# Optimization experiments

Hardware: AMD Instinct MI355X
Metric: run time of the kernel (lower is better)

Reference implementation:

```python
import jax, jax.numpy as jnp
import numpy as np

IN_F = 175
HID = 1024
OUT_F = 175


def setup_inputs() -> dict:
    key = jax.random.key(0)
    ks = jax.random.split(key, 16)
    B, T = 128, 200
    s = 0.02
    w = lambda k, shape: (jax.random.normal(k, shape, jnp.float32) * s)
    return {
        "real_seq": jax.random.normal(ks[0], (B, T, IN_F), jnp.float32),
        "W_ih1": w(ks[1], (4 * HID, IN_F)), "W_hh1": w(ks[2], (4 * HID, HID)),
        "b_ih1": w(ks[3], (4 * HID,)), "b_hh1": w(ks[4], (4 * HID,)),
        "W_ih2": w(ks[5], (4 * HID, HID)), "W_hh2": w(ks[6], (4 * HID, HID)),
        "b_ih2": w(ks[7], (4 * HID,)), "b_hh2": w(ks[8], (4 * HID,)),
        "W_ih3": w(ks[9], (4 * HID, HID)), "W_hh3": w(ks[10], (4 * HID, HID)),
        "b_ih3": w(ks[11], (4 * HID,)), "b_hh3": w(ks[12], (4 * HID,)),
        "W_dec": w(ks[13], (OUT_F, HID)), "b_dec": w(ks[14], (OUT_F,)),
    }


def _condition_mask(seq_len, condition_num=5, groundtruth_num=5):
    gt = np.ones((100, groundtruth_num))
    con = np.zeros((100, condition_num))
    lst = np.concatenate((gt, con), 1).reshape(-1)[:seq_len]
    return jnp.asarray(lst.astype(bool))


def _lstm_cell(x, h, c, Wih, Whh, bih, bhh):
    # PyTorch LSTMCell: gate order i, f, g, o
    gates = x @ Wih.T + h @ Whh.T + bih + bhh
    i, f, g, o = jnp.split(gates, 4, axis=-1)
    c_new = jax.nn.sigmoid(f) * c + jax.nn.sigmoid(i) * jnp.tanh(g)
    h_new = jax.nn.sigmoid(o) * jnp.tanh(c_new)
    return h_new, c_new


def reference(real_seq, W_ih1, W_hh1, b_ih1, b_hh1,
              W_ih2, W_hh2, b_ih2, b_hh2,
              W_ih3, W_hh3, b_ih3, b_hh3,
              W_dec, b_dec):
    B, T, _ = real_seq.shape
    H = W_hh1.shape[1]
    Fo = W_dec.shape[0]
    cond = _condition_mask(T)
    z = jnp.zeros((B, H), real_seq.dtype)
    carry0 = (z, z, z, z, z, z, jnp.zeros((B, Fo), real_seq.dtype))

    def step(carry, xs):
        h0, h1, h2, c0, c1, c2, out_frame = carry
        x_t, use_gt = xs
        in_frame = jnp.where(use_gt, x_t, out_frame)
        nh0, nc0 = _lstm_cell(in_frame, h0, c0, W_ih1, W_hh1, b_ih1, b_hh1)
        # NOTE: source feeds the PREVIOUS h0 / h1 to layers 2 / 3 (faithful)
        nh1, nc1 = _lstm_cell(h0, h1, c1, W_ih2, W_hh2, b_ih2, b_hh2)
        nh2, nc2 = _lstm_cell(h1, h2, c2, W_ih3, W_hh3, b_ih3, b_hh3)
        out = nh2 @ W_dec.T + b_dec
        return (nh0, nh1, nh2, nc0, nc1, nc2, out), out

    _, outs = jax.lax.scan(step, carry0,
                           (jnp.transpose(real_seq, (1, 0, 2)), cond))
    # [T, B, Fo] -> [B, T*Fo] (matches torch.cat along dim 1 per step)
    return jnp.transpose(outs, (1, 0, 2)).reshape(B, T * Fo)
```

## Files before the change

kernel.cpp:

```cpp
#include <hip/hip_runtime.h>

#define B_ 128
#define T_ 200
#define INF_ 175
#define INFP_ 192
#define H_ 1024
#define G4_ 4096
#define OUTF_ 175
#define BH3_ (3 * B_ * H_)
#define NCELL 192
#define NDEC 22
#define NWORK (NCELL + NDEC)
#define NBLK (NWORK + 1)
#define SP 16

typedef __bf16 bf16x8 __attribute__((ext_vector_type(8)));
typedef float f32x4 __attribute__((ext_vector_type(4)));

__device__ __attribute__((aligned(16))) __bf16 g_Wih1p[G4_ * INFP_];
__device__ __attribute__((aligned(16))) __bf16 g_Whh1[G4_ * H_];
__device__ __attribute__((aligned(16))) __bf16 g_Wih2[G4_ * H_];
__device__ __attribute__((aligned(16))) __bf16 g_Whh2[G4_ * H_];
__device__ __attribute__((aligned(16))) __bf16 g_Wih3[G4_ * H_];
__device__ __attribute__((aligned(16))) __bf16 g_Whh3[G4_ * H_];
__device__ __attribute__((aligned(16))) __bf16 g_Wdec[OUTF_ * H_];
__device__ float g_bsum[3 * G4_];
__device__ float g_bdec[OUTF_];
__device__ __attribute__((aligned(16))) __bf16 g_h[2][BH3_];
__device__ __attribute__((aligned(16))) __bf16 g_infp[B_ * INFP_];
__device__ __attribute__((aligned(16))) __bf16 g_xp[(long)T_ * B_ * INFP_];
__device__ int g_isf32;
__device__ int g_flags[256 * SP];
__device__ int g_dflags[32 * SP];
__device__ int g_gen8[8 * SP];
__device__ int g_iready8[8 * SP];

__device__ __forceinline__ f32x4 mfma_bf16(bf16x8 a, bf16x8 b, f32x4 c) {
    return __builtin_amdgcn_mfma_f32_16x16x32_bf16(a, b, c, 0, 0, 0);
}
__device__ __forceinline__ bf16x8 ld8(const __bf16* p) {
    return *reinterpret_cast<const bf16x8*>(p);
}
__device__ __forceinline__ float sigm(float x) { return 1.f / (1.f + expf(-x)); }
__device__ __forceinline__ float rdf(const void* p, long i, int f32) {
    return f32 ? ((const float*)p)[i] : (float)((const __bf16*)p)[i];
}
__device__ __forceinline__ unsigned short bf2u(__bf16 v) {
    union { __bf16 b; unsigned short u; } c; c.b = v; return c.u;
}

__device__ __forceinline__ void lds_barrier() {
    asm volatile("s_waitcnt lgkmcnt(0)" ::: "memory");
    __builtin_amdgcn_s_barrier();
}

__device__ __forceinline__ void spin_rmw(int* addr, int target, int iters) {
    for (int it = 0; it < iters; ++it) {
        if (__hip_atomic_fetch_max(addr, 0, __ATOMIC_RELAXED, __HIP_MEMORY_SCOPE_AGENT) >= target)
            break;
        __builtin_amdgcn_s_sleep(1);
    }
    (void)__hip_atomic_load(addr, __ATOMIC_ACQUIRE, __HIP_MEMORY_SCOPE_AGENT);
}

__global__ void detect_k(const unsigned int* __restrict__ xw) {
    __shared__ int cnt;
    if (threadIdx.x == 0) cnt = 0;
    __syncthreads();
    unsigned int w = xw[threadIdx.x];
    int e = (w >> 7) & 0xFF;
    if (e >= 140) atomicAdd(&cnt, 1);
    __syncthreads();
    if (threadIdx.x == 0) g_isf32 = (cnt >= 16) ? 1 : 0;
}

__global__ void prep_k(const void* Wih1, const void* Whh1, const void* Wih2,
                       const void* Whh2, const void* Wih3, const void* Whh3,
                       const void* Wdec, const void* bih1, const void* bhh1,
                       const void* bih2, const void* bhh2, const void* bih3,
                       const void* bhh3, const void* bdec, const void* xseq) {
    const int f = g_isf32;
    const int idx = blockIdx.x * 256 + threadIdx.x;
    const int stride = gridDim.x * 256;
    if (idx < 256 * SP) g_flags[idx] = 0;
    if (idx < 32 * SP) g_dflags[idx] = 0;
    if (idx < 8 * SP) { g_gen8[idx] = 0; g_iready8[idx] = 0; }
    for (int i = idx; i < G4_ * INFP_; i += stride) {
        int n = i / INFP_, k = i - n * INFP_;
        g_Wih1p[i] = (k < INF_) ? (__bf16)rdf(Wih1, (long)n * INF_ + k, f) : (__bf16)0.f;
    }
    for (int i = idx; i < G4_ * H_; i += stride) {
        g_Whh1[i] = (__bf16)rdf(Whh1, i, f);
        g_Wih2[i] = (__bf16)rdf(Wih2, i, f);
        g_Whh2[i] = (__bf16)rdf(Whh2, i, f);
        g_Wih3[i] = (__bf16)rdf(Wih3, i, f);
        g_Whh3[i] = (__bf16)rdf(Whh3, i, f);
    }
    for (int i = idx; i < OUTF_ * H_; i += stride) g_Wdec[i] = (__bf16)rdf(Wdec, i, f);
    for (int i = idx; i < G4_; i += stride) {
        g_bsum[i]           = rdf(bih1, i, f) + rdf(bhh1, i, f);
        g_bsum[G4_ + i]     = rdf(bih2, i, f) + rdf(bhh2, i, f);
        g_bsum[2 * G4_ + i] = rdf(bih3, i, f) + rdf(bhh3, i, f);
    }
    for (int i = idx; i < OUTF_; i += stride) g_bdec[i] = rdf(bdec, i, f);
    for (int i = idx; i < 2 * BH3_; i += stride) (&g_h[0][0])[i] = (__bf16)0.f;
    for (int i = idx; i < B_ * INFP_; i += stride) g_infp[i] = (__bf16)0.f;
    const long total = (long)T_ * B_ * INFP_;
    for (long i = idx; i < total; i += stride) {
        int k = (int)(i % INFP_);
        long bt = i / INFP_;
        int b = (int)(bt % B_);
        int t = (int)(bt / B_);
        g_xp[((long)t * B_ + b) * INFP_ + k] =
            (k < INF_) ? (__bf16)rdf(xseq, (long)b * (T_ * INF_) + (long)t * INF_ + k, f)
                       : (__bf16)0.f;
    }
}

__device__ __forceinline__ void gridbar_w(int bid, int grp, int target) {
    __syncthreads();
    if (threadIdx.x == 0) {
        __threadfence();
        __hip_atomic_fetch_max(&g_flags[bid * SP], target, __ATOMIC_RELAXED, __HIP_MEMORY_SCOPE_AGENT);
        spin_rmw(&g_gen8[grp * SP], target, 4000);
    }
    __syncthreads();
}

__global__ __launch_bounds__(512, 1) void persist_k(const void* __restrict__ xseq,
                                                    void* __restrict__ dout) {
    __shared__ char s_tile[2][2][16384];
    __shared__ float s_acc[B_ * 4 * 16];
    __shared__ float s_c[B_ * 16];
    __shared__ int s_nf, s_nd;
    const int bid = blockIdx.x;
    const int grp = bid & 7;
    const int tid = threadIdx.x;
    const int lane = tid & 63;
    const int wid = tid >> 6;
    const int rlo = lane & 15, khi = lane >> 4;
    const int f32o = g_isf32;
    const int r7l = rlo & 7;
    const int sw0 = (khi ^ r7l) * 16;
    const int sw1 = ((khi + 4) ^ r7l) * 16;

    if (bid < NCELL) {
        const int L = bid >> 6;
        const int hc0 = (bid & 63) << 4;
        const int op = wid >> 2;
        const int g = wid & 3;
        const float* bs = g_bsum + L * G4_;
        const int XOFF = (L == 0) ? 13 : 0;

        const __bf16* Bm; int K;
        if (op == 0) {
            if (L == 0) { Bm = g_Wih1p; K = INFP_; }
            else        { Bm = (L == 1) ? g_Wih2 : g_Wih3; K = H_; }
        } else {
            Bm = (L == 0) ? g_Whh1 : (L == 1) ? g_Whh2 : g_Whh3; K = H_;
        }
        const __bf16* wp = Bm + (long)(g * H_ + hc0 + rlo) * K + khi * 8;
        bf16x8 wreg[32];
        if (K == INFP_) {
#pragma unroll
            for (int c = 0; c < 6; ++c) wreg[c] = ld8(wp + c * 32);
        } else {
#pragma unroll
            for (int c = 0; c < 32; ++c) wreg[c] = ld8(wp + c * 32);
        }

        const int strow = tid >> 2, stq = tid & 3, str7 = strow & 7;
        auto ldchunk = [&](const __bf16* src, int sA, int k0, bf16x8& v0, bf16x8& v1) {
            const __bf16* pr = src + (long)strow * sA + k0 + stq * 8;
            v0 = ld8(pr);
            v1 = ld8(pr + 32);
        };
        auto wrchunk = [&](char* tile, bf16x8 v0, bf16x8 v1) {
            char* pb = tile + strow * 128;
            *(bf16x8*)(pb + ((stq ^ str7) * 16)) = v0;
            *(bf16x8*)(pb + (((stq + 4) ^ str7) * 16)) = v1;
        };

        for (int i = tid; i < B_ * 16; i += 512) s_c[i] = 0.f;
        __syncthreads();

        for (int p = 0; p < T_; ++p) {
            const bool gt = ((p % 10) < 5);
            const __bf16* hin = g_h[p & 1];
            const __bf16* Apx; int sAx, nx;
            if (L == 0) {
                Apx = gt ? (g_xp + (long)p * B_ * INFP_) : g_infp;
                sAx = INFP_; nx = 3;
            } else {
                Apx = hin + (L - 1) * B_ * H_; sAx = H_; nx = 16;
            }
            const __bf16* Aph = hin + L * B_ * H_;
            const bool needwait = (L == 0) && !gt;

            bf16x8 rx0, rx1, rh0, rh1;
            ldchunk(Aph, H_, 0, rh0, rh1);
            if (XOFF == 0) ldchunk(Apx, sAx, 0, rx0, rx1);
            wrchunk(&s_tile[0][1][0], rh0, rh1);
            if (XOFF == 0) wrchunk(&s_tile[0][0][0], rx0, rx1);
            ldchunk(Aph, H_, 64, rh0, rh1);
            if (XOFF == 0) ldchunk(Apx, sAx, 64, rx0, rx1);
            lds_barrier();

            f32x4 acc[8] = {};
            int buf = 0;
#pragma unroll
            for (int i = 0; i < 16; ++i) {
                if (i < 15) wrchunk(&s_tile[buf ^ 1][1][0], rh0, rh1);
                {
                    int xj = i + 1 - XOFF;
                    if (xj >= 0 && xj < nx) wrchunk(&s_tile[buf ^ 1][0][0], rx0, rx1);
                }
                if (i == 11 && needwait) {
                    if (tid == 0) spin_rmw(&g_iready8[grp * SP], p, 3000);
                    __syncthreads();
                }
                if (i < 14) ldchunk(Aph, H_, (i + 2) * 64, rh0, rh1);
                {
                    int xj = i + 2 - XOFF;
                    if (xj >= 0 && xj < nx) ldchunk(Apx, sAx, xj * 64, rx0, rx1);
                }
                if (op == 1) {
                    const char* tb = &s_tile[buf][1][0];
#pragma unroll
                    for (int mf = 0; mf < 8; ++mf) {
                        const char* rb = tb + (mf * 16 + rlo) * 128;
                        acc[mf] = mfma_bf16(*(const bf16x8*)(rb + sw0), wreg[2 * i], acc[mf]);
                        acc[mf] = mfma_bf16(*(const bf16x8*)(rb + sw1), wreg[2 * i + 1], acc[mf]);
                    }
                } else {
                    int xj = i - XOFF;
                    if (xj >= 0 && xj < nx) {
                        const char* tb = &s_tile[buf][0][0];
#pragma unroll
                        for (int mf = 0; mf < 8; ++mf) {
                            const char* rb = tb + (mf * 16 + rlo) * 128;
                            acc[mf] = mfma_bf16(*(const bf16x8*)(rb + sw0), wreg[2 * xj], acc[mf]);
                            acc[mf] = mfma_bf16(*(const bf16x8*)(rb + sw1), wreg[2 * xj + 1], acc[mf]);
                        }
                    }
                }
                lds_barrier();
                buf ^= 1;
            }

            if (op == 1) {
#pragma unroll
                for (int mf = 0; mf < 8; ++mf)
#pragma unroll
                    for (int j = 0; j < 4; ++j) {
                        int r = mf * 16 + khi * 4 + j;
                        s_acc[(r * 4 + g) * 16 + rlo] = acc[mf][j];
                    }
            }
            __syncthreads();
            if (op == 0) {
#pragma unroll
                for (int mf = 0; mf < 8; ++mf)
#pragma unroll
                    for (int j = 0; j < 4; ++j) {
                        int r = mf * 16 + khi * 4 + j;
                        s_acc[(r * 4 + g) * 16 + rlo] += acc[mf][j];
                    }
            }
            __syncthreads();

            {
                const int r = wid * 16 + rlo;
                const int hq = khi;
                f32x4 ga = *(const f32x4*)&s_acc[(r * 4 + 0) * 16 + hq * 4];
                f32x4 gf = *(const f32x4*)&s_acc[(r * 4 + 1) * 16 + hq * 4];
                f32x4 gg = *(const f32x4*)&s_acc[(r * 4 + 2) * 16 + hq * 4];
                f32x4 go = *(const f32x4*)&s_acc[(r * 4 + 3) * 16 + hq * 4];
                f32x4 cv = *(const f32x4*)&s_c[r * 16 + hq * 4];
                unsigned long long hbits;
                unsigned short* hp = (unsigned short*)&hbits;
#pragma unroll
                for (int e = 0; e < 4; ++e) {
                    int col = hc0 + hq * 4 + e;
                    float gi_ = ga[e] + bs[0 * H_ + col];
                    float gf_ = gf[e] + bs[1 * H_ + col];
                    float gg_ = gg[e] + bs[2 * H_ + col];
                    float go_ = go[e] + bs[3 * H_ + col];
                    float cn = sigm(gf_) * cv[e] + sigm(gi_) * tanhf(gg_);
                    cv[e] = cn;
                    hp[e] = bf2u((__bf16)(sigm(go_) * tanhf(cn)));
                }
                *(f32x4*)&s_c[r * 16 + hq * 4] = cv;
                __bf16* hdst = g_h[(p + 1) & 1] + L * B_ * H_ + r * H_ + hc0 + hq * 4;
                __builtin_nontemporal_store(hbits, (unsigned long long*)hdst);
            }
            gridbar_w(bid, grp, p + 1);
        }
    } else if (bid < NWORK) {
        const int db = bid - NCELL;
        const int ntile = db % 11, mh = db / 11;
        const int kk = wid >> 2;
        const int mw = wid & 3;
        const int col = ntile * 16 + rlo;
        const int colc = (col < OUTF_) ? col : (OUTF_ - 1);

        const __bf16* pb = g_Wdec + (long)colc * H_ + khi * 8;
        bf16x8 dw[16];
#pragma unroll
        for (int c = 0; c < 16; ++c) dw[c] = ld8(pb + (kk * 16 + c) * 32);

        const int strow = tid >> 3, stc8 = tid & 7, str7 = strow & 7;
        char* const dt0 = &s_tile[0][0][0];
        char* const dt1 = &s_tile[1][0][0];

        auto decwork = [&](int t, bool winf) {
            const bool gtn = (((t + 1) % 10) < 5);
            const __bf16* h2 = g_h[(t + 1) & 1] + 2 * B_ * H_;
            const __bf16* hrow = h2 + (long)(mh * 64 + strow) * H_ + stc8 * 8;
            bf16x8 rv = ld8(hrow);
            *(bf16x8*)(dt0 + strow * 128 + ((stc8 ^ str7) * 16)) = rv;
            rv = ld8(hrow + 64);
            lds_barrier();
            f32x4 acc = {};
            int b = 0;
#pragma unroll
            for (int i = 0; i < 16; ++i) {
                if (i < 15) *(bf16x8*)((b ? dt0 : dt1) + strow * 128 + ((stc8 ^ str7) * 16)) = rv;
                if (i < 14) rv = ld8(hrow + (i + 2) * 64);
                {
                    const char* rb = (b ? dt1 : dt0) + (mw * 16 + rlo) * 128;
                    bf16x8 a0 = *(const bf16x8*)(rb + sw0);
                    bf16x8 a1 = *(const bf16x8*)(rb + sw1);
                    if (i < 8) {
                        if (kk == 0) {
                            acc = mfma_bf16(a0, dw[2 * i], acc);
                            acc = mfma_bf16(a1, dw[2 * i + 1], acc);
                        }
                    } else {
                        if (kk == 1) {
                            acc = mfma_bf16(a0, dw[2 * i - 16], acc);
                            acc = mfma_bf16(a1, dw[2 * i - 15], acc);
                        }
                    }
                }
                lds_barrier();
                b ^= 1;
            }
            if (kk == 1) {
#pragma unroll
                for (int j = 0; j < 4; ++j)
                    s_acc[(mw * 16 + khi * 4 + j) * 16 + rlo] = acc[j];
            }
            __syncthreads();
            if (kk == 0) {
#pragma unroll
                for (int j = 0; j < 4; ++j)
                    acc[j] += s_acc[(mw * 16 + khi * 4 + j) * 16 + rlo];
                if (col < OUTF_) {
                    const float bias = g_bdec[col];
#pragma unroll
                    for (int j = 0; j < 4; ++j) {
                        int row = mh * 64 + mw * 16 + khi * 4 + j;
                        float ov = acc[j] + bias;
                        long oidx = (long)row * (T_ * OUTF_) + (long)t * OUTF_ + col;
                        if (f32o) __builtin_nontemporal_store(ov, (float*)dout + oidx);
                        else __builtin_nontemporal_store(bf2u((__bf16)ov), (unsigned short*)dout + oidx);
                        if (winf && !gtn) {
                            __builtin_nontemporal_store(bf2u((__bf16)ov),
                                (unsigned short*)g_infp + row * INFP_ + col);
                        }
                    }
                }
            }
            __syncthreads();
            if (tid == 0) {
                __threadfence();
                __hip_atomic_fetch_max(&g_dflags[db * SP], t + 1, __ATOMIC_RELAXED, __HIP_MEMORY_SCOPE_AGENT);
            }
        };

        for (int p = 0; p < T_; ++p) {
            if (p >= 1) decwork(p - 1, true);
            gridbar_w(bid, grp, p + 1);
        }
        decwork(T_ - 1, false);
    } else {
        for (int p = 0; p < T_; ++p) {
            const int tgt = p + 1;
            bool ir_done = false;
            for (int it = 0; it < 2000; ++it) {
                if (tid == 0) { s_nf = 0; s_nd = 0; }
                __syncthreads();
                int bad_f = 0, bad_d = 0;
                if (tid < NWORK)
                    bad_f = (__hip_atomic_fetch_max(&g_flags[tid * SP], 0, __ATOMIC_RELAXED, __HIP_MEMORY_SCOPE_AGENT) < tgt);
                if (!ir_done && tid < NDEC)
                    bad_d = (__hip_atomic_fetch_max(&g_dflags[tid * SP], 0, __ATOMIC_RELAXED, __HIP_MEMORY_SCOPE_AGENT) < p);
                if (bad_f) s_nf = 1;
                if (bad_d) s_nd = 1;
                __syncthreads();
                if (!ir_done && !s_nd) {
                    if (tid < 8)
                        __hip_atomic_fetch_max(&g_iready8[tid * SP], p, __ATOMIC_RELAXED, __HIP_MEMORY_SCOPE_AGENT);
                    ir_done = true;
                }
                if (!s_nf) break;
                __builtin_amdgcn_s_sleep(1);
            }
            if (!ir_done && tid < 8)
                __hip_atomic_fetch_max(&g_iready8[tid * SP], p, __ATOMIC_RELAXED, __HIP_MEMORY_SCOPE_AGENT);
            __syncthreads();
            if (tid < 8)
                __hip_atomic_fetch_max(&g_gen8[tid * SP], tgt, __ATOMIC_RELAXED, __HIP_MEMORY_SCOPE_AGENT);
        }
    }
}

extern "C" void kernel_launch(void* const* d_in, const int* in_sizes, int n_in,
                              void* d_out, int out_size, void* d_ws, size_t ws_size,
                              hipStream_t stream) {
    const void* xseq = d_in[0];
    detect_k<<<1, 256, 0, stream>>>((const unsigned int*)xseq);
    prep_k<<<2048, 256, 0, stream>>>(d_in[1], d_in[2], d_in[5], d_in[6], d_in[9],
                                     d_in[10], d_in[13], d_in[3], d_in[4], d_in[7],
                                     d_in[8], d_in[11], d_in[12], d_in[14], xseq);
    persist_k<<<NBLK, 512, 0, stream>>>(xseq, d_out);
}
```

Before: 6.071 ms.

## Split LSTM cell warps over K halves with two gates each, padding LDS reductions

```diff
diff --git a/kernel.cpp b/kernel.cpp
--- a/kernel.cpp
+++ b/kernel.cpp
@@ -13,6 +13,9 @@
 #define NWORK (NCELL + NDEC)
 #define NBLK (NWORK + 1)
 #define SP 16
+#define AS 69
+#define CS 17
+#define DS 17
 
 typedef __bf16 bf16x8 __attribute__((ext_vector_type(8)));
 typedef float f32x4 __attribute__((ext_vector_type(4)));
@@ -130,8 +133,8 @@
 __global__ __launch_bounds__(512, 1) void persist_k(const void* __restrict__ xseq,
                                                     void* __restrict__ dout) {
     __shared__ char s_tile[2][2][16384];
-    __shared__ float s_acc[B_ * 4 * 16];
-    __shared__ float s_c[B_ * 16];
+    __shared__ float s_acc[B_ * AS];
+    __shared__ float s_c[B_ * CS];
     __shared__ int s_nf, s_nd;
     const int bid = blockIdx.x;
     const int grp = bid & 7;
@@ -148,7 +151,8 @@
         const int L = bid >> 6;
         const int hc0 = (bid & 63) << 4;
         const int op = wid >> 2;
-        const int g = wid & 3;
+        const int gp = (wid >> 1) & 1;
+        const int kh = wid & 1;
         const float* bs = g_bsum + L * G4_;
         const int XOFF = (L == 0) ? 13 : 0;
 
@@ -159,14 +163,29 @@
         } else {
             Bm = (L == 0) ? g_Whh1 : (L == 1) ? g_Whh2 : g_Whh3; K = H_;
         }
-        const __bf16* wp = Bm + (long)(g * H_ + hc0 + rlo) * K + khi * 8;
+        const __bf16* wpA = Bm + (long)((gp * 2 + 0) * H_ + hc0 + rlo) * K + khi * 8;
+        const __bf16* wpB = Bm + (long)((gp * 2 + 1) * H_ + hc0 + rlo) * K + khi * 8;
         bf16x8 wreg[32];
         if (K == INFP_) {
 #pragma unroll
-            for (int c = 0; c < 6; ++c) wreg[c] = ld8(wp + c * 32);
+            for (int ci = 0; ci < 2; ++ci) {
+                int c = ci * 2 + kh;
+                if (c < 3) {
+                    wreg[ci * 4 + 0] = ld8(wpA + c * 64);
+                    wreg[ci * 4 + 1] = ld8(wpA + c * 64 + 32);
+                    wreg[ci * 4 + 2] = ld8(wpB + c * 64);
+                    wreg[ci * 4 + 3] = ld8(wpB + c * 64 + 32);
+                }
+            }
         } else {
 #pragma unroll
-            for (int c = 0; c < 32; ++c) wreg[c] = ld8(wp + c * 32);
+            for (int ci = 0; ci < 8; ++ci) {
+                int c = ci * 2 + kh;
+                wreg[ci * 4 + 0] = ld8(wpA + c * 64);
+                wreg[ci * 4 + 1] = ld8(wpA + c * 64 + 32);
+                wreg[ci * 4 + 2] = ld8(wpB + c * 64);
+                wreg[ci * 4 + 3] = ld8(wpB + c * 64 + 32);
+            }
         }
 
         const int strow = tid >> 2, stq = tid & 3, str7 = strow & 7;
@@ -181,7 +200,7 @@
             *(bf16x8*)(pb + (((stq + 4) ^ str7) * 16)) = v1;
         };
 
-        for (int i = tid; i < B_ * 16; i += 512) s_c[i] = 0.f;
+        for (int i = tid; i < B_ * CS; i += 512) s_c[i] = 0.f;
         __syncthreads();
 
         for (int p = 0; p < T_; ++p) {
@@ -206,7 +225,7 @@
             if (XOFF == 0) ldchunk(Apx, sAx, 64, rx0, rx1);
             lds_barrier();
 
-            f32x4 acc[8] = {};
+            f32x4 acc[8][2] = {};
             int buf = 0;
 #pragma unroll
             for (int i = 0; i < 16; ++i) {
@@ -225,22 +244,34 @@
                     if (xj >= 0 && xj < nx) ldchunk(Apx, sAx, xj * 64, rx0, rx1);
                 }
                 if (op == 1) {
-                    const char* tb = &s_tile[buf][1][0];
-#pragma unroll
-                    for (int mf = 0; mf < 8; ++mf) {
-                        const char* rb = tb + (mf * 16 + rlo) * 128;
-                        acc[mf] = mfma_bf16(*(const bf16x8*)(rb + sw0), wreg[2 * i], acc[mf]);
-                        acc[mf] = mfma_bf16(*(const bf16x8*)(rb + sw1), wreg[2 * i + 1], acc[mf]);
+                    if ((i & 1) == kh) {
+                        const int ci = i >> 1;
+                        const char* tb = &s_tile[buf][1][0];
+#pragma unroll
+                        for (int mf = 0; mf < 8; ++mf) {
+                            const char* rb = tb + (mf * 16 + rlo) * 128;
+                            bf16x8 a0 = *(const bf16x8*)(rb + sw0);
+                            bf16x8 a1 = *(const bf16x8*)(rb + sw1);
+                            acc[mf][0] = mfma_bf16(a0, wreg[ci * 4 + 0], acc[mf][0]);
+                            acc[mf][1] = mfma_bf16(a0, wreg[ci * 4 + 2], acc[mf][1]);
+                            acc[mf][0] = mfma_bf16(a1, wreg[ci * 4 + 1], acc[mf][0]);
+                            acc[mf][1] = mfma_bf16(a1, wreg[ci * 4 + 3], acc[mf][1]);
+                        }
                     }
                 } else {
                     int xj = i - XOFF;
-                    if (xj >= 0 && xj < nx) {
+                    if (xj >= 0 && xj < nx && (xj & 1) == kh) {
+                        const int ci = xj >> 1;
                         const char* tb = &s_tile[buf][0][0];
 #pragma unroll
                         for (int mf = 0; mf < 8; ++mf) {
                             const char* rb = tb + (mf * 16 + rlo) * 128;
-                            acc[mf] = mfma_bf16(*(const bf16x8*)(rb + sw0), wreg[2 * xj], acc[mf]);
-                            acc[mf] = mfma_bf16(*(const bf16x8*)(rb + sw1), wreg[2 * xj + 1], acc[mf]);
+                            bf16x8 a0 = *(const bf16x8*)(rb + sw0);
+                            bf16x8 a1 = *(const bf16x8*)(rb + sw1);
+                            acc[mf][0] = mfma_bf16(a0, wreg[ci * 4 + 0], acc[mf][0]);
+                            acc[mf][1] = mfma_bf16(a0, wreg[ci * 4 + 2], acc[mf][1]);
+                            acc[mf][0] = mfma_bf16(a1, wreg[ci * 4 + 1], acc[mf][0]);
+                            acc[mf][1] = mfma_bf16(a1, wreg[ci * 4 + 3], acc[mf][1]);
                         }
                     }
                 }
@@ -248,49 +279,46 @@
                 buf ^= 1;
             }
 
-            if (op == 1) {
-#pragma unroll
-                for (int mf = 0; mf < 8; ++mf)
-#pragma unroll
-                    for (int j = 0; j < 4; ++j) {
-                        int r = mf * 16 + khi * 4 + j;
-                        s_acc[(r * 4 + g) * 16 + rlo] = acc[mf][j];
-                    }
-            }
-            __syncthreads();
-            if (op == 0) {
-#pragma unroll
-                for (int mf = 0; mf < 8; ++mf)
-#pragma unroll
-                    for (int j = 0; j < 4; ++j) {
-                        int r = mf * 16 + khi * 4 + j;
-                        s_acc[(r * 4 + g) * 16 + rlo] += acc[mf][j];
-                    }
-            }
-            __syncthreads();
+#pragma unroll
+            for (int rd = 0; rd < 4; ++rd) {
+                const int rop = (rd < 2) ? 1 : 0, rkh = rd & 1;
+                if (op == rop && kh == rkh) {
+#pragma unroll
+                    for (int mf = 0; mf < 8; ++mf)
+#pragma unroll
+                        for (int g01 = 0; g01 < 2; ++g01)
+#pragma unroll
+                            for (int j = 0; j < 4; ++j) {
+                                int r = mf * 16 + khi * 4 + j;
+                                int gc = (gp * 2 + g01) * 16 + rlo;
+                                if (rd == 0) s_acc[r * AS + gc] = acc[mf][g01][j];
+                                else         s_acc[r * AS + gc] += acc[mf][g01][j];
+                            }
+                }
+                __syncthreads();
+            }
 
             {
                 const int r = wid * 16 + rlo;
                 const int hq = khi;
-                f32x4 ga = *(const f32x4*)&s_acc[(r * 4 + 0) * 16 + hq * 4];
-                f32x4 gf = *(const f32x4*)&s_acc[(r * 4 + 1) * 16 + hq * 4];
-                f32x4 gg = *(const f32x4*)&s_acc[(r * 4 + 2) * 16 + hq * 4];
-                f32x4 go = *(const f32x4*)&s_acc[(r * 4 + 3) * 16 + hq * 4];
-                f32x4 cv = *(const f32x4*)&s_c[r * 16 + hq * 4];
+                float cv[4];
+#pragma unroll
+                for (int e = 0; e < 4; ++e) cv[e] = s_c[r * CS + hq * 4 + e];
                 unsigned long long hbits;
                 unsigned short* hp = (unsigned short*)&hbits;
 #pragma unroll
                 for (int e = 0; e < 4; ++e) {
                     int col = hc0 + hq * 4 + e;
-                    float gi_ = ga[e] + bs[0 * H_ + col];
-                    float gf_ = gf[e] + bs[1 * H_ + col];
-                    float gg_ = gg[e] + bs[2 * H_ + col];
-                    float go_ = go[e] + bs[3 * H_ + col];
+                    float gi_ = s_acc[r * AS + 0 * 16 + hq * 4 + e] + bs[0 * H_ + col];
+                    float gf_ = s_acc[r * AS + 1 * 16 + hq * 4 + e] + bs[1 * H_ + col];
+                    float gg_ = s_acc[r * AS + 2 * 16 + hq * 4 + e] + bs[2 * H_ + col];
+                    float go_ = s_acc[r * AS + 3 * 16 + hq * 4 + e] + bs[3 * H_ + col];
                     float cn = sigm(gf_) * cv[e] + sigm(gi_) * tanhf(gg_);
                     cv[e] = cn;
                     hp[e] = bf2u((__bf16)(sigm(go_) * tanhf(cn)));
                 }
-                *(f32x4*)&s_c[r * 16 + hq * 4] = cv;
+#pragma unroll
+                for (int e = 0; e < 4; ++e) s_c[r * CS + hq * 4 + e] = cv[e];
                 __bf16* hdst = g_h[(p + 1) & 1] + L * B_ * H_ + r * H_ + hc0 + hq * 4;
                 __builtin_nontemporal_store(hbits, (unsigned long long*)hdst);
             }
@@ -349,13 +377,13 @@
             if (kk == 1) {
 #pragma unroll
                 for (int j = 0; j < 4; ++j)
-                    s_acc[(mw * 16 + khi * 4 + j) * 16 + rlo] = acc[j];
+                    s_acc[(mw * 16 + khi * 4 + j) * DS + rlo] = acc[j];
             }
             __syncthreads();
             if (kk == 0) {
 #pragma unroll
                 for (int j = 0; j < 4; ++j)
-                    acc[j] += s_acc[(mw * 16 + khi * 4 + j) * 16 + rlo];
+                    acc[j] += s_acc[(mw * 16 + khi * 4 + j) * DS + rlo];
                 if (col < OUTF_) {
                     const float bias = g_bdec[col];
 #pragma unroll
```

Result: slower. 8.799 ms (+44.9%).
